# Performance work log

Hardware: AMD Instinct MI355X
Metric: run time of the kernel (lower is better)

## Reference

```python
import jax, jax.numpy as jnp
import numpy as np

NUM_CLASSES = 21
FEAT_DIM = 256
TEMP = 0.1
EPS = 1e-12  # F.normalize default eps


def setup_inputs() -> dict:
    key = jax.random.key(0)
    k1, k2, k3, k4 = jax.random.split(key, 4)
    H = W = 768
    features = jax.random.normal(k1, (1, FEAT_DIM, H, W), dtype=jnp.float32)
    prototypes = jax.random.normal(k2, (NUM_CLASSES, FEAT_DIM), dtype=jnp.float32)
    outputs = jax.random.normal(k3, (1, NUM_CLASSES, H, W), dtype=jnp.float32)
    labels = jax.random.randint(k4, (1, 1, H, W), 0, NUM_CLASSES, dtype=jnp.int32)
    return {"features": features, "prototypes": prototypes, "outputs": outputs, "labels": labels}


def reference(features, prototypes, outputs, labels):
    # features: [1, D, H, W]; prototypes: [C, D]; labels: [1, 1, H, W]
    B, D, H, W = features.shape
    C = prototypes.shape[0]
    # Per-pixel feature vectors [N, D] (batch=1, matching torch's view(D, -1) semantics)
    f = features[0].reshape(D, H * W).T
    # F.normalize(features_cl, p=2, dim=0): unit-normalize each pixel's feature vector
    norm = jnp.linalg.norm(f, axis=1, keepdims=True)
    fn = f / jnp.maximum(norm, EPS)
    lab = labels.reshape(-1)  # [N]
    # Per-class mean of normalized features (scatter-mean); all C classes present
    sums = jax.ops.segment_sum(fn, lab, num_segments=C)  # [C, D]
    counts = jax.ops.segment_sum(jnp.ones(lab.shape, dtype=fn.dtype), lab, num_segments=C)  # [C]
    features_local_mean = sums / jnp.maximum(counts, 1.0)[:, None]
    # Prototype logits + masked contrastive loss over classes 1..C-1
    logits = (features_local_mean @ prototypes.T) / TEMP  # [C, C]
    shifted = logits - jnp.max(logits, axis=1, keepdims=True)
    denom = jnp.sum(jnp.exp(shifted[1:, 1:]), axis=1)  # [C-1]
    numer_log = jnp.diagonal(shifted)[1:]  # shifted[cl, cl] for cl in 1..C-1
    loss = jnp.mean(jnp.log(denom) - numer_log)
    return loss
```

## Files before the change

kernel.cpp:

```cpp
#include <hip/hip_runtime.h>
#include <math.h>

#define FEAT_DIM 256
#define NCLS 21
#define TEMP 0.1f
#define NREP 8

typedef float f32x4  __attribute__((ext_vector_type(4)));
typedef float f32x16 __attribute__((ext_vector_type(16)));
typedef int   i32x4  __attribute__((ext_vector_type(4)));
typedef unsigned int u32x4 __attribute__((ext_vector_type(4)));
typedef short bf16x8 __attribute__((ext_vector_type(8)));

__device__ __forceinline__ unsigned int cvt_pk_bf16(float lo, float hi) {
    unsigned int r;
    asm("v_cvt_pk_bf16_f32 %0, %1, %2" : "=v"(r) : "v"(lo), "v"(hi));
    return r;
}

template <int CTRL>
__device__ __forceinline__ float dpp_add(float x) {
    int y = __builtin_amdgcn_update_dpp(
        0, __builtin_bit_cast(int, x), CTRL, 0xF, 0xF, true);
    return x + __builtin_bit_cast(float, y);
}
__device__ __forceinline__ float sum16(float x) {
    x = dpp_add<0xB1>(x);
    x = dpp_add<0x4E>(x);
    x = dpp_add<0x141>(x);
    x = dpp_add<0x128>(x);
    return x;
}

__global__ __launch_bounds__(512, 2)
void k_fused(const float* __restrict__ feat, const int* __restrict__ lab,
             float* __restrict__ gsum, float* __restrict__ gcnt, int N) {
    __shared__ float s_ssp[8][2][32];
    __shared__ float s_ivf[32];
    __shared__ int   s_lab[32];

    const int tid = threadIdx.x, lane = tid & 63, w = tid >> 6;
    const int half = lane >> 5, ch = lane & 31;
    const int ntile = N / (gridDim.x * 32);
    const size_t px0 = (size_t)blockIdx.x * ntile * 32;

    const float* fbase = feat + (size_t)(w * 32 + ch) * (size_t)N + px0 + half * 8;

    f32x16 acc = 0.0f;
    float cntacc = 0.f;
    float4 VA[4], VB[4], VC3[4];
    int labA = 0, labB = 0, labC = 0;

    if (w == 1) labA = lab[px0 + (lane & 31)];
    #pragma unroll
    for (int j = 0; j < 4; ++j)
        VA[j] = *reinterpret_cast<const float4*>(fbase + (j >> 1) * 16 + (j & 1) * 4);
    if (w == 1) labB = lab[px0 + 32 + (lane & 31)];
    #pragma unroll
    for (int j = 0; j < 4; ++j)
        VB[j] = *reinterpret_cast<const float4*>(fbase + 32 + (j >> 1) * 16 + (j & 1) * 4);

    auto process = [&](int t, float4 (&VC)[4], int labc,
                       float4 (&VN2)[4], int& labn2) {
        if (t + 2 < ntile) {
            if (w == 1) labn2 = lab[px0 + (size_t)(t + 2) * 32 + (lane & 31)];
            const float* fn_ = fbase + (size_t)(t + 2) * 32;
            #pragma unroll
            for (int j = 0; j < 4; ++j)
                VN2[j] = *reinterpret_cast<const float4*>(fn_ + (j >> 1) * 16 + (j & 1) * 4);
        }
        #pragma unroll
        for (int c = 0; c < 2; ++c) {
            const float4 v0 = VC[2 * c], v1 = VC[2 * c + 1];
            const float s0 = sum16(v0.x * v0.x);
            const float s1 = sum16(v0.y * v0.y);
            const float s2 = sum16(v0.z * v0.z);
            const float s3 = sum16(v0.w * v0.w);
            const float s4 = sum16(v1.x * v1.x);
            const float s5 = sum16(v1.y * v1.y);
            const float s6 = sum16(v1.z * v1.z);
            const float s7 = sum16(v1.w * v1.w);
            if ((lane & 15) == 0) {
                float* b = &s_ssp[w][(lane >> 4) & 1][c * 16 + half * 8];
                *reinterpret_cast<f32x4*>(b)     = (f32x4){s0, s1, s2, s3};
                *reinterpret_cast<f32x4*>(b + 4) = (f32x4){s4, s5, s6, s7};
            }
        }
        asm volatile("s_waitcnt lgkmcnt(0)" ::: "memory");
        __builtin_amdgcn_s_barrier();

        if (w == 0 && lane < 32) {
            float ss = 0.f;
            #pragma unroll
            for (int q = 0; q < 8; ++q)
                ss += s_ssp[q][0][lane] + s_ssp[q][1][lane];
            s_ivf[lane] = 1.0f / fmaxf(sqrtf(ss), 1e-12f);
        }
        if (w == 1 && lane < 32) s_lab[lane] = labc;
        asm volatile("s_waitcnt lgkmcnt(0)" ::: "memory");
        __builtin_amdgcn_s_barrier();

        #pragma unroll
        for (int c = 0; c < 2; ++c) {
            const int o = c * 16 + half * 8;
            const i32x4 lb0 = *reinterpret_cast<const i32x4*>(&s_lab[o]);
            const i32x4 lb1 = *reinterpret_cast<const i32x4*>(&s_lab[o + 4]);
            const f32x4 iv0 = *reinterpret_cast<const f32x4*>(&s_ivf[o]);
            const f32x4 iv1 = *reinterpret_cast<const f32x4*>(&s_ivf[o + 4]);
            const float4 v0 = VC[2 * c], v1 = VC[2 * c + 1];
            u32x4 bw, aw;
            bw[0] = cvt_pk_bf16(v0.x * iv0[0], v0.y * iv0[1]);
            bw[1] = cvt_pk_bf16(v0.z * iv0[2], v0.w * iv0[3]);
            bw[2] = cvt_pk_bf16(v1.x * iv1[0], v1.y * iv1[1]);
            bw[3] = cvt_pk_bf16(v1.z * iv1[2], v1.w * iv1[3]);
            aw[0] = (lb0[0] == ch ? 0x3F80u : 0u) | (lb0[1] == ch ? 0x3F800000u : 0u);
            aw[1] = (lb0[2] == ch ? 0x3F80u : 0u) | (lb0[3] == ch ? 0x3F800000u : 0u);
            aw[2] = (lb1[0] == ch ? 0x3F80u : 0u) | (lb1[1] == ch ? 0x3F800000u : 0u);
            aw[3] = (lb1[2] == ch ? 0x3F80u : 0u) | (lb1[3] == ch ? 0x3F800000u : 0u);
            acc = __builtin_amdgcn_mfma_f32_32x32x16_bf16(
                __builtin_bit_cast(bf16x8, aw),
                __builtin_bit_cast(bf16x8, bw), acc, 0, 0, 0);
        }

        if (w == 1) {
            #pragma unroll 1
            for (int c = 0; c < NCLS; ++c) {
                const unsigned long long m =
                    __ballot(labc == c) & 0xFFFFFFFFull;
                if (lane == c) cntacc += (float)__popcll(m);
            }
        }
    };

    for (int t = 0; t < ntile; t += 3) {
        process(t,     VA,  labA, VC3, labC);
        process(t + 1, VB,  labB, VA,  labA);
        process(t + 2, VC3, labC, VB,  labB);
    }

    {
        float* grep = gsum + (size_t)(blockIdx.x & (NREP - 1)) * (NCLS * FEAT_DIM);
        const int dcol = w * 32 + ch;
        #pragma unroll
        for (int r = 0; r < 16; ++r) {
            const int row = (r & 3) + 8 * (r >> 2) + 4 * half;
            if (row < NCLS) atomicAdd(&grep[row * FEAT_DIM + dcol], acc[r]);
        }
    }
    if (w == 1 && lane < NCLS) atomicAdd(&gcnt[lane], cntacc);
}

__global__ void k_final(const float* __restrict__ gsum,
                        const float* __restrict__ gcnt,
                        const float* __restrict__ proto,
                        float* __restrict__ out) {
    __shared__ float s_mean[NCLS * 257];
    __shared__ float s_icnt[NCLS];
    __shared__ float s_log[NCLS * NCLS];
    __shared__ float s_term[NCLS];

    if (threadIdx.x < NCLS)
        s_icnt[threadIdx.x] = 1.0f / fmaxf(gcnt[threadIdx.x], 1.0f);
    __syncthreads();

    for (int i = threadIdx.x; i < NCLS * FEAT_DIM; i += blockDim.x) {
        float v = 0.f;
        #pragma unroll
        for (int r = 0; r < NREP; ++r) v += gsum[r * NCLS * FEAT_DIM + i];
        const int c = i / FEAT_DIM, d = i - c * FEAT_DIM;
        s_mean[c * 257 + d] = v * s_icnt[c];
    }
    __syncthreads();

    for (int p = threadIdx.x; p < NCLS * NCLS; p += blockDim.x) {
        const int c = p / NCLS, j = p - c * NCLS;
        float acc = 0.f;
        #pragma unroll 8
        for (int d = 0; d < FEAT_DIM; ++d)
            acc += s_mean[c * 257 + d] * proto[j * FEAT_DIM + d];
        s_log[p] = acc / TEMP;
    }
    __syncthreads();

    if (threadIdx.x >= 1 && threadIdx.x < NCLS) {
        const int c = threadIdx.x;
        float m = -INFINITY;
        for (int j = 0; j < NCLS; ++j) m = fmaxf(m, s_log[c * NCLS + j]);
        float den = 0.f;
        for (int j = 1; j < NCLS; ++j) den += expf(s_log[c * NCLS + j] - m);
        s_term[c] = logf(den) - (s_log[c * NCLS + c] - m);
    }
    __syncthreads();

    if (threadIdx.x == 0) {
        float acc = 0.f;
        for (int c = 1; c < NCLS; ++c) acc += s_term[c];
        out[0] = acc / (float)(NCLS - 1);
    }
}

extern "C" void kernel_launch(void* const* d_in, const int* in_sizes, int n_in,
                              void* d_out, int out_size, void* d_ws, size_t ws_size,
                              hipStream_t stream) {
    const float* feat  = (const float*)d_in[0];
    const float* proto = (const float*)d_in[1];
    const int*   lab   = (const int*)d_in[3];

    const int N = in_sizes[3];

    float* gsum = (float*)d_ws;
    float* gcnt = gsum + NREP * NCLS * FEAT_DIM;

    (void)hipMemsetAsync(gsum, 0,
                         (NREP * NCLS * FEAT_DIM + NCLS) * sizeof(float), stream);

    k_fused<<<512, 512, 0, stream>>>(feat, lab, gsum, gcnt, N);
    k_final<<<1, 256, 0, stream>>>(gsum, gcnt, proto, (float*)d_out);
}
```

Before: 166.7 us.

## Remove second barrier per tile by computing norms redundantly per wave

New measurement: 207.4 us. 24.4% more time.

```diff
diff --git a/kernel.cpp b/kernel.cpp
--- a/kernel.cpp
+++ b/kernel.cpp
@@ -35,9 +35,8 @@
 __global__ __launch_bounds__(512, 2)
 void k_fused(const float* __restrict__ feat, const int* __restrict__ lab,
              float* __restrict__ gsum, float* __restrict__ gcnt, int N) {
-    __shared__ float s_ssp[8][2][32];
-    __shared__ float s_ivf[32];
-    __shared__ int   s_lab[32];
+    __shared__ float s_ssp[2][8][2][32];
+    __shared__ float s_ivf[8][32];
 
     const int tid = threadIdx.x, lane = tid & 63, w = tid >> 6;
     const int half = lane >> 5, ch = lane & 31;
@@ -49,21 +48,17 @@
     f32x16 acc = 0.0f;
     float cntacc = 0.f;
     float4 VA[4], VB[4], VC3[4];
-    int labA = 0, labB = 0, labC = 0;
-
-    if (w == 1) labA = lab[px0 + (lane & 31)];
+
     #pragma unroll
     for (int j = 0; j < 4; ++j)
         VA[j] = *reinterpret_cast<const float4*>(fbase + (j >> 1) * 16 + (j & 1) * 4);
-    if (w == 1) labB = lab[px0 + 32 + (lane & 31)];
     #pragma unroll
     for (int j = 0; j < 4; ++j)
         VB[j] = *reinterpret_cast<const float4*>(fbase + 32 + (j >> 1) * 16 + (j & 1) * 4);
 
-    auto process = [&](int t, float4 (&VC)[4], int labc,
-                       float4 (&VN2)[4], int& labn2) {
+    auto process = [&](int t, float4 (&VC)[4], float4 (&VN2)[4]) {
+        const int par = t & 1;
         if (t + 2 < ntile) {
-            if (w == 1) labn2 = lab[px0 + (size_t)(t + 2) * 32 + (lane & 31)];
             const float* fn_ = fbase + (size_t)(t + 2) * 32;
             #pragma unroll
             for (int j = 0; j < 4; ++j)
@@ -81,7 +76,7 @@
             const float s6 = sum16(v1.z * v1.z);
             const float s7 = sum16(v1.w * v1.w);
             if ((lane & 15) == 0) {
-                float* b = &s_ssp[w][(lane >> 4) & 1][c * 16 + half * 8];
+                float* b = &s_ssp[par][w][(lane >> 4) & 1][c * 16 + half * 8];
                 *reinterpret_cast<f32x4*>(b)     = (f32x4){s0, s1, s2, s3};
                 *reinterpret_cast<f32x4*>(b + 4) = (f32x4){s4, s5, s6, s7};
             }
@@ -89,53 +84,57 @@
         asm volatile("s_waitcnt lgkmcnt(0)" ::: "memory");
         __builtin_amdgcn_s_barrier();
 
-        if (w == 0 && lane < 32) {
-            float ss = 0.f;
-            #pragma unroll
-            for (int q = 0; q < 8; ++q)
-                ss += s_ssp[q][0][lane] + s_ssp[q][1][lane];
-            s_ivf[lane] = 1.0f / fmaxf(sqrtf(ss), 1e-12f);
-        }
-        if (w == 1 && lane < 32) s_lab[lane] = labc;
-        asm volatile("s_waitcnt lgkmcnt(0)" ::: "memory");
-        __builtin_amdgcn_s_barrier();
+        const int* lb = lab + px0 + (size_t)t * 32;
+        const i32x4 lf0a = *reinterpret_cast<const i32x4*>(lb + half * 8);
+        const i32x4 lf0b = *reinterpret_cast<const i32x4*>(lb + half * 8 + 4);
+        const i32x4 lf1a = *reinterpret_cast<const i32x4*>(lb + 16 + half * 8);
+        const i32x4 lf1b = *reinterpret_cast<const i32x4*>(lb + 16 + half * 8 + 4);
+        const int   labl = lb[ch];
+
+        float ss = 0.f;
+        #pragma unroll
+        for (int q = 0; q < 8; ++q)
+            ss += s_ssp[par][q][0][ch] + s_ssp[par][q][1][ch];
+        const float ivl = 1.0f / fmaxf(sqrtf(ss), 1e-12f);
+        if (lane < 32) s_ivf[w][lane] = ivl;
 
         #pragma unroll
         for (int c = 0; c < 2; ++c) {
             const int o = c * 16 + half * 8;
-            const i32x4 lb0 = *reinterpret_cast<const i32x4*>(&s_lab[o]);
-            const i32x4 lb1 = *reinterpret_cast<const i32x4*>(&s_lab[o + 4]);
-            const f32x4 iv0 = *reinterpret_cast<const f32x4*>(&s_ivf[o]);
-            const f32x4 iv1 = *reinterpret_cast<const f32x4*>(&s_ivf[o + 4]);
+            const i32x4 la = (c == 0) ? lf0a : lf1a;
+            const i32x4 lbv = (c == 0) ? lf0b : lf1b;
+            const f32x4 iv0 = *reinterpret_cast<const f32x4*>(&s_ivf[w][o]);
+            const f32x4 iv1 = *reinterpret_cast<const f32x4*>(&s_ivf[w][o + 4]);
             const float4 v0 = VC[2 * c], v1 = VC[2 * c + 1];
             u32x4 bw, aw;
             bw[0] = cvt_pk_bf16(v0.x * iv0[0], v0.y * iv0[1]);
             bw[1] = cvt_pk_bf16(v0.z * iv0[2], v0.w * iv0[3]);
             bw[2] = cvt_pk_bf16(v1.x * iv1[0], v1.y * iv1[1]);
             bw[3] = cvt_pk_bf16(v1.z * iv1[2], v1.w * iv1[3]);
-            aw[0] = (lb0[0] == ch ? 0x3F80u : 0u) | (lb0[1] == ch ? 0x3F800000u : 0u);
-            aw[1] = (lb0[2] == ch ? 0x3F80u : 0u) | (lb0[3] == ch ? 0x3F800000u : 0u);
-            aw[2] = (lb1[0] == ch ? 0x3F80u : 0u) | (lb1[1] == ch ? 0x3F800000u : 0u);
-            aw[3] = (lb1[2] == ch ? 0x3F80u : 0u) | (lb1[3] == ch ? 0x3F800000u : 0u);
+            aw[0] = (la[0]  == ch ? 0x3F80u : 0u) | (la[1]  == ch ? 0x3F800000u : 0u);
+            aw[1] = (la[2]  == ch ? 0x3F80u : 0u) | (la[3]  == ch ? 0x3F800000u : 0u);
+            aw[2] = (lbv[0] == ch ? 0x3F80u : 0u) | (lbv[1] == ch ? 0x3F800000u : 0u);
+            aw[3] = (lbv[2] == ch ? 0x3F80u : 0u) | (lbv[3] == ch ? 0x3F800000u : 0u);
             acc = __builtin_amdgcn_mfma_f32_32x32x16_bf16(
                 __builtin_bit_cast(bf16x8, aw),
                 __builtin_bit_cast(bf16x8, bw), acc, 0, 0, 0);
         }
 
-        if (w == 1) {
-            #pragma unroll 1
-            for (int c = 0; c < NCLS; ++c) {
+        #pragma unroll
+        for (int k = 0; k < 3; ++k) {
+            const int c = w + 8 * k;
+            if (c < NCLS) {
                 const unsigned long long m =
-                    __ballot(labc == c) & 0xFFFFFFFFull;
+                    __ballot(labl == c) & 0xFFFFFFFFull;
                 if (lane == c) cntacc += (float)__popcll(m);
             }
         }
     };
 
     for (int t = 0; t < ntile; t += 3) {
-        process(t,     VA,  labA, VC3, labC);
-        process(t + 1, VB,  labB, VA,  labA);
-        process(t + 2, VC3, labC, VB,  labB);
+        process(t,     VA,  VC3);
+        process(t + 1, VB,  VA);
+        process(t + 2, VC3, VB);
     }
 
     {
@@ -147,7 +146,7 @@
             if (row < NCLS) atomicAdd(&grep[row * FEAT_DIM + dcol], acc[r]);
         }
     }
-    if (w == 1 && lane < NCLS) atomicAdd(&gcnt[lane], cntacc);
+    if (lane < NCLS && (lane & 7) == w) atomicAdd(&gcnt[lane], cntacc);
 }
 
 __global__ void k_final(const float* __restrict__ gsum,
```
